# Kernel tuning notes

Hardware: AMD Instinct MI355X
Metric: run time of the kernel (lower is better)

Reference implementation:

```python
import jax, jax.numpy as jnp
import numpy as np
import math

NUM_HEADS = 16
VEC_SIZE = 1024
HEAD_DIM = VEC_SIZE // NUM_HEADS


def setup_inputs() -> dict:
    key = jax.random.key(0)
    k1, k2, k3, k4, k5 = jax.random.split(key, 5)
    B, S, D = 2, 2048, VEC_SIZE
    x = jax.random.normal(k1, (B, S, D), dtype=jnp.float32)
    # Linear params, torch-style: y = x @ W.T + b
    s1 = 1.0 / math.sqrt(D)
    W_qkv = jax.random.uniform(k2, (3 * D, D), minval=-s1, maxval=s1, dtype=jnp.float32)
    b_qkv = jax.random.uniform(k3, (3 * D,), minval=-s1, maxval=s1, dtype=jnp.float32)
    W_out = jax.random.uniform(k4, (D, D), minval=-s1, maxval=s1, dtype=jnp.float32)
    b_out = jax.random.uniform(k5, (D,), minval=-s1, maxval=s1, dtype=jnp.float32)
    return {"x": x, "W_qkv": W_qkv, "b_qkv": b_qkv, "W_out": W_out, "b_out": b_out}


def reference(x, W_qkv, b_qkv, W_out, b_out):
    B, S, D = x.shape
    H, Hd = NUM_HEADS, HEAD_DIM
    qkv = x @ W_qkv.T + b_qkv                      # [B,S,3D]
    q, k, v = jnp.split(qkv, 3, axis=-1)
    # [B,S,H,Hd] -> [B,H,S,Hd]
    q = q.reshape(B, S, H, Hd).transpose(0, 2, 1, 3)
    k = k.reshape(B, S, H, Hd).transpose(0, 2, 1, 3)
    v = v.reshape(B, S, H, Hd).transpose(0, 2, 1, 3)
    weight = jnp.einsum('bhqd,bhkd->bhqk', q, k)   # [B,H,S,S]
    causal = jnp.triu(jnp.ones((S, S), dtype=bool), k=1)
    weight = jnp.where(causal, -jnp.inf, weight)
    weight = weight / jnp.sqrt(jnp.asarray(Hd, dtype=weight.dtype))
    weight = jax.nn.softmax(weight, axis=-1)
    out = jnp.einsum('bhqk,bhkd->bhqd', weight, v)  # [B,H,S,Hd]
    out = out.transpose(0, 2, 1, 3).reshape(B, S, D)
    return out @ W_out.T + b_out
```

## Files before the change

kernel.cpp:

```cpp
#include <hip/hip_runtime.h>
#include <hip/hip_bf16.h>

typedef __attribute__((ext_vector_type(8))) short short8;
typedef __attribute__((ext_vector_type(4))) short s4v;
typedef __attribute__((ext_vector_type(4))) float floatx4;

__device__ inline floatx4 mfma_bf16(short8 a, short8 b, floatx4 c) {
  return __builtin_amdgcn_mfma_f32_16x16x32_bf16(a, b, c, 0, 0, 0);
}
__device__ inline float exp2_fast(float x) { return __builtin_amdgcn_exp2f(x); }

__device__ inline short bf16s(float f) {
  __hip_bfloat16 h = __float2bfloat16(f);
  return *reinterpret_cast<short*>(&h);
}
__device__ inline float sbf16(short s) {
  return __bfloat162float(*reinterpret_cast<__hip_bfloat16*>(&s));
}

__device__ inline void gld16(__hip_bfloat16* lds, const __hip_bfloat16* g) {
  __builtin_amdgcn_global_load_lds(
      (const __attribute__((address_space(1))) void*)g,
      (__attribute__((address_space(3))) void*)lds, 16, 0, 0);
}

__global__ __launch_bounds__(256) void cvt_all(
    const float* __restrict__ x, const float* __restrict__ wqkv,
    const float* __restrict__ wout, __hip_bfloat16* __restrict__ xb,
    __hip_bfloat16* __restrict__ wqkvb, __hip_bfloat16* __restrict__ wob) {
  const int n1 = 4194304, n2 = 3145728;
  int i = (blockIdx.x * 256 + threadIdx.x) * 8;
  const float* src;
  __hip_bfloat16* dst;
  int off;
  if (i < n1) { src = x; dst = xb; off = i; }
  else if (i < n1 + n2) { src = wqkv; dst = wqkvb; off = i - n1; }
  else { src = wout; dst = wob; off = i - n1 - n2; }
  float4 a = *reinterpret_cast<const float4*>(src + off);
  float4 b = *reinterpret_cast<const float4*>(src + off + 4);
  __hip_bfloat16 t[8];
  t[0] = __float2bfloat16(a.x); t[1] = __float2bfloat16(a.y);
  t[2] = __float2bfloat16(a.z); t[3] = __float2bfloat16(a.w);
  t[4] = __float2bfloat16(b.x); t[5] = __float2bfloat16(b.y);
  t[6] = __float2bfloat16(b.z); t[7] = __float2bfloat16(b.w);
  *reinterpret_cast<short8*>(dst + off) = *reinterpret_cast<short8*>(t);
}

template<int TN, bool OUT_BF16>
__global__ __launch_bounds__(256) void gemm_bt(
    const __hip_bfloat16* __restrict__ A, const __hip_bfloat16* __restrict__ Bt,
    const float* __restrict__ bias, void* __restrict__ Cout,
    int M, int N, int K) {
  __shared__ __align__(16) __hip_bfloat16 As[128 * 64];
  __shared__ __align__(16) __hip_bfloat16 Bs[TN * 64];
  const int tid = threadIdx.x;
  const int wave = tid >> 6, lane = tid & 63, quad = lane >> 4, l15 = lane & 15;
  const int wm = (wave >> 1) * 64, wn = (wave & 1) * (TN / 2);
  const int m0 = blockIdx.y * 128, n0 = blockIdx.x * TN;
  const int NC = TN / 32;

  floatx4 acc[4][NC];
  for (int r = 0; r < 4; ++r)
    for (int c = 0; c < NC; ++c) acc[r][c] = (floatx4){0.f, 0.f, 0.f, 0.f};

  for (int k0 = 0; k0 < K; k0 += 64) {
    __syncthreads();
    for (int it = 0; it < 4; ++it) {
      int idx = it * 256 + tid;
      int row = idx >> 3, col = ((idx & 7) ^ (row & 7)) * 8;
      gld16(&As[idx * 8], A + (size_t)(m0 + row) * K + k0 + col);
    }
    for (int it = 0; it < TN * 64 / 2048; ++it) {
      int idx = it * 256 + tid;
      int row = idx >> 3, col = ((idx & 7) ^ (row & 7)) * 8;
      gld16(&Bs[idx * 8], Bt + (size_t)(n0 + row) * K + k0 + col);
    }
    __syncthreads();
    for (int ks = 0; ks < 2; ++ks) {
      short8 af[4], bf[NC];
      for (int r = 0; r < 4; ++r) {
        int row = wm + r * 16 + l15;
        af[r] = *reinterpret_cast<const short8*>(
            &As[row * 64 + (((ks * 4 + quad) ^ (l15 & 7)) * 8)]);
      }
      for (int c = 0; c < NC; ++c) {
        int row = wn + c * 16 + l15;
        bf[c] = *reinterpret_cast<const short8*>(
            &Bs[row * 64 + (((ks * 4 + quad) ^ (l15 & 7)) * 8)]);
      }
      for (int r = 0; r < 4; ++r)
        for (int c = 0; c < NC; ++c)
          acc[r][c] = mfma_bf16(af[r], bf[c], acc[r][c]);
    }
  }

  for (int c = 0; c < NC; ++c) {
    int gn = n0 + wn + c * 16 + l15;
    float bv = bias[gn];
    for (int r = 0; r < 4; ++r)
      for (int rg = 0; rg < 4; ++rg) {
        int gm = m0 + wm + r * 16 + quad * 4 + rg;
        float v = acc[r][c][rg] + bv;
        if (OUT_BF16)
          ((__hip_bfloat16*)Cout)[(size_t)gm * N + gn] = __float2bfloat16(v);
        else
          ((float*)Cout)[(size_t)gm * N + gn] = v;
      }
  }
}

__global__ __launch_bounds__(256, 4) void flash_attn(
    const __hip_bfloat16* __restrict__ qkv, __hip_bfloat16* __restrict__ out) {
  const int S = 2048, QKV = 3072;
  const int bx = blockIdx.x;
  const int g = (blockIdx.y >> 3) + 2 * blockIdx.z;
  int qt;
  if (g == 0)      qt = bx;
  else if (g == 1) qt = 31 - bx;
  else if (g == 2) qt = (bx + 8) & 31;
  else             qt = (23 - bx) & 31;
  const int h = blockIdx.y, b = blockIdx.z;
  const int q0 = qt * 64;
  __shared__ __align__(16) short Ps[64 * 64];
  __shared__ __align__(16) short Ks[2][64 * 64];
  __shared__ __align__(16) short Vts[2][64 * 64];
  const int tid = threadIdx.x;
  const int wave = tid >> 6, lane = tid & 63, quad = lane >> 4, l15 = lane & 15;
  const int rx = l15 & 7;
  const __hip_bfloat16* base = qkv + (size_t)b * S * QKV;
  const float c2 = 0.18033688011112042f;
  const floatx4 zero4 = {0.f, 0.f, 0.f, 0.f};

  const int j4 = (tid >> 4) * 4, d4 = (tid & 15) * 4;

  for (int it = 0; it < 2; ++it) {
    int v = tid + it * 256;
    int row = v >> 3, cb = v & 7;
    int colp = (cb ^ (row & 7)) * 8;
    gld16((__hip_bfloat16*)&Ks[0][v * 8],
          base + (size_t)row * QKV + 1024 + h * 64 + colp);
    short8 qv = *reinterpret_cast<const short8*>(
        base + (size_t)(q0 + row) * QKV + h * 64 + cb * 8);
    short qs[8];
    for (int e = 0; e < 8; ++e) qs[e] = bf16s(sbf16(qv[e]) * c2);
    *reinterpret_cast<short8*>(&Ps[row * 64 + colp]) = *reinterpret_cast<short8*>(qs);
  }
  {
    s4v vr[4];
    for (int jj = 0; jj < 4; ++jj)
      vr[jj] = *reinterpret_cast<const s4v*>(
          base + (size_t)(j4 + jj) * QKV + 2048 + h * 64 + d4);
    for (int e = 0; e < 4; ++e) {
      int d = d4 + e;
      int pb = (j4 >> 3) ^ (d & 7) ^ ((d >> 3) & 7);
      s4v w4 = {vr[0][e], vr[1][e], vr[2][e], vr[3][e]};
      *reinterpret_cast<s4v*>(&Vts[0][d * 64 + pb * 8 + (j4 & 7)]) = w4;
    }
  }
  __syncthreads();
  short8 aq[4][2];
  for (int t4 = 0; t4 < 4; ++t4)
    for (int s = 0; s < 2; ++s)
      aq[t4][s] = *reinterpret_cast<const short8*>(
          &Ps[(t4 * 16 + l15) * 64 + (((s * 4 + quad) ^ rx) * 8)]);
  __syncthreads();

  floatx4 o_acc[4];
  for (int m = 0; m < 4; ++m) o_acc[m] = zero4;
  float lsum4[4] = {0.f, 0.f, 0.f, 0.f};
  const int krow = 16 * wave + l15;

  for (int kt = 0; kt <= qt; ++kt) {
    const int cur = kt & 1, nb = cur ^ 1;
    const bool havenext = kt < qt;
    s4v vr[4];
    if (havenext) {
      const size_t r1 = (size_t)(kt + 1) * 64;
      for (int it = 0; it < 2; ++it) {
        int v = tid + it * 256;
        int row = v >> 3, cb = v & 7;
        int colp = (cb ^ (row & 7)) * 8;
        gld16((__hip_bfloat16*)&Ks[nb][v * 8],
              base + (r1 + row) * QKV + 1024 + h * 64 + colp);
      }
      for (int jj = 0; jj < 4; ++jj)
        vr[jj] = *reinterpret_cast<const s4v*>(
            base + (r1 + j4 + jj) * QKV + 2048 + h * 64 + d4);
    }

    short8 ak0 = *reinterpret_cast<const short8*>(
        &Ks[cur][krow * 64 + ((quad ^ rx) * 8)]);
    short8 ak1 = *reinterpret_cast<const short8*>(
        &Ks[cur][krow * 64 + (((4 + quad) ^ rx) * 8)]);
    floatx4 sc[4];
    for (int t4 = 0; t4 < 4; ++t4) {
      sc[t4] = mfma_bf16(ak0, aq[t4][0], zero4);
      sc[t4] = mfma_bf16(ak1, aq[t4][1], sc[t4]);
    }
    if (kt == qt) {
      int kloc = 16 * wave + quad * 4;
      for (int t4 = 0; t4 < 4; ++t4)
        for (int rg = 0; rg < 4; ++rg)
          if (kloc + rg > t4 * 16 + l15) sc[t4][rg] = -1e30f;
    }
    const int pcol = ((2 * wave + (quad >> 1)) ^ rx) * 8 + (quad & 1) * 4;
    for (int t4 = 0; t4 < 4; ++t4) {
      short pp[4];
      for (int rg = 0; rg < 4; ++rg) {
        float p = exp2_fast(sc[t4][rg]);
        lsum4[t4] += p;
        pp[rg] = bf16s(p);
      }
      *reinterpret_cast<s4v*>(&Ps[(t4 * 16 + l15) * 64 + pcol]) =
          *reinterpret_cast<s4v*>(pp);
    }
    __syncthreads();

    const int dg = 16 * wave + l15;
    for (int s = 0; s < 2; ++s) {
      int gsw = ((4 * s + quad) ^ (dg & 7) ^ ((dg >> 3) & 7)) * 8;
      short8 bv = *reinterpret_cast<const short8*>(&Vts[cur][dg * 64 + gsw]);
      for (int m = 0; m < 4; ++m) {
        short8 ap = *reinterpret_cast<const short8*>(
            &Ps[(m * 16 + l15) * 64 + (((4 * s + quad) ^ rx) * 8)]);
        o_acc[m] = mfma_bf16(ap, bv, o_acc[m]);
      }
    }

    if (havenext) {
      for (int e = 0; e < 4; ++e) {
        int d = d4 + e;
        int pb = (j4 >> 3) ^ (d & 7) ^ ((d >> 3) & 7);
        s4v w4 = {vr[0][e], vr[1][e], vr[2][e], vr[3][e]};
        *reinterpret_cast<s4v*>(&Vts[nb][d * 64 + pb * 8 + (j4 & 7)]) = w4;
      }
    }
    __syncthreads();
  }

  for (int t4 = 0; t4 < 4; ++t4) {
    lsum4[t4] += __shfl_xor(lsum4[t4], 16);
    lsum4[t4] += __shfl_xor(lsum4[t4], 32);
  }
  float* Lf = (float*)Ps;
  if (quad == 0)
    for (int t4 = 0; t4 < 4; ++t4)
      Lf[wave * 64 + t4 * 16 + l15] = lsum4[t4];
  __syncthreads();
  if (tid < 64)
    Lf[256 + tid] = 1.0f / (Lf[tid] + Lf[64 + tid] + Lf[128 + tid] + Lf[192 + tid]);
  __syncthreads();

  const int dcol = h * 64 + 16 * wave + l15;
  for (int m = 0; m < 4; ++m)
    for (int rg = 0; rg < 4; ++rg) {
      int q = m * 16 + quad * 4 + rg;
      float inv = Lf[256 + q];
      out[(size_t)(b * S + q0 + q) * 1024 + dcol] =
          __float2bfloat16(o_acc[m][rg] * inv);
    }
}

extern "C" void kernel_launch(void* const* d_in, const int* in_sizes, int n_in,
                              void* d_out, int out_size, void* d_ws, size_t ws_size,
                              hipStream_t stream) {
  const float* x    = (const float*)d_in[0];
  const float* Wqkv = (const float*)d_in[1];
  const float* bqkv = (const float*)d_in[2];
  const float* Wout = (const float*)d_in[3];
  const float* bout = (const float*)d_in[4];
  float* out = (float*)d_out;

  const int BS = 2 * 2048;
  const int D = 1024;
  char* ws = (char*)d_ws;
  __hip_bfloat16* xb    = (__hip_bfloat16*)(ws);
  __hip_bfloat16* wqkvb = (__hip_bfloat16*)(ws + (size_t)8  * 1048576);
  __hip_bfloat16* wob   = (__hip_bfloat16*)(ws + (size_t)14 * 1048576);
  __hip_bfloat16* qkvb  = (__hip_bfloat16*)(ws + (size_t)16 * 1048576);
  __hip_bfloat16* attnb = (__hip_bfloat16*)(ws + (size_t)40 * 1048576);

  cvt_all<<<4096, 256, 0, stream>>>(x, Wqkv, Wout, xb, wqkvb, wob);

  gemm_bt<128, true><<<dim3(3072 / 128, BS / 128), 256, 0, stream>>>(
      xb, wqkvb, bqkv, qkvb, BS, 3 * D, D);

  flash_attn<<<dim3(32, 16, 2), 256, 0, stream>>>(qkvb, attnb);

  gemm_bt<64, false><<<dim3(1024 / 64, BS / 128), 256, 0, stream>>>(
      attnb, wob, bout, out, BS, D, D);
}
```

Baseline: 188.8 us.

## Software-pipeline flash attention: overlap PV of previous tile with QK of current

Restructures the attention loop so the P·V product for tile j-1 runs alongside the QK^T and softmax of tile j. Ps is double-buffered, and the V transpose write to LDS is deferred by one iteration. This cuts the per-iteration barriers from two to one and lets the scheduler interleave the two matrix phases. In exchange it uses more LDS and registers, so launch_bounds occupancy drops from 4 to 3 blocks per CU.

```diff
diff --git a/kernel.cpp b/kernel.cpp
--- a/kernel.cpp
+++ b/kernel.cpp
@@ -109,7 +109,7 @@
   }
 }
 
-__global__ __launch_bounds__(256, 4) void flash_attn(
+__global__ __launch_bounds__(256, 3) void flash_attn(
     const __hip_bfloat16* __restrict__ qkv, __hip_bfloat16* __restrict__ out) {
   const int S = 2048, QKV = 3072;
   const int bx = blockIdx.x;
@@ -121,7 +121,7 @@
   else             qt = (23 - bx) & 31;
   const int h = blockIdx.y, b = blockIdx.z;
   const int q0 = qt * 64;
-  __shared__ __align__(16) short Ps[64 * 64];
+  __shared__ __align__(16) short Ps[2][64 * 64];
   __shared__ __align__(16) short Ks[2][64 * 64];
   __shared__ __align__(16) short Vts[2][64 * 64];
   const int tid = threadIdx.x;
@@ -130,7 +130,6 @@
   const __hip_bfloat16* base = qkv + (size_t)b * S * QKV;
   const float c2 = 0.18033688011112042f;
   const floatx4 zero4 = {0.f, 0.f, 0.f, 0.f};
-
   const int j4 = (tid >> 4) * 4, d4 = (tid & 15) * 4;
 
   for (int it = 0; it < 2; ++it) {
@@ -143,66 +142,72 @@
         base + (size_t)(q0 + row) * QKV + h * 64 + cb * 8);
     short qs[8];
     for (int e = 0; e < 8; ++e) qs[e] = bf16s(sbf16(qv[e]) * c2);
-    *reinterpret_cast<short8*>(&Ps[row * 64 + colp]) = *reinterpret_cast<short8*>(qs);
-  }
-  {
-    s4v vr[4];
-    for (int jj = 0; jj < 4; ++jj)
-      vr[jj] = *reinterpret_cast<const s4v*>(
-          base + (size_t)(j4 + jj) * QKV + 2048 + h * 64 + d4);
-    for (int e = 0; e < 4; ++e) {
-      int d = d4 + e;
-      int pb = (j4 >> 3) ^ (d & 7) ^ ((d >> 3) & 7);
-      s4v w4 = {vr[0][e], vr[1][e], vr[2][e], vr[3][e]};
-      *reinterpret_cast<s4v*>(&Vts[0][d * 64 + pb * 8 + (j4 & 7)]) = w4;
-    }
-  }
+    *reinterpret_cast<short8*>(&Ps[1][row * 64 + colp]) = *reinterpret_cast<short8*>(qs);
+  }
+  s4v vr[4];
+  for (int jj = 0; jj < 4; ++jj)
+    vr[jj] = *reinterpret_cast<const s4v*>(
+        base + (size_t)(j4 + jj) * QKV + 2048 + h * 64 + d4);
   __syncthreads();
+
   short8 aq[4][2];
   for (int t4 = 0; t4 < 4; ++t4)
     for (int s = 0; s < 2; ++s)
       aq[t4][s] = *reinterpret_cast<const short8*>(
-          &Ps[(t4 * 16 + l15) * 64 + (((s * 4 + quad) ^ rx) * 8)]);
-  __syncthreads();
+          &Ps[1][(t4 * 16 + l15) * 64 + (((s * 4 + quad) ^ rx) * 8)]);
 
   floatx4 o_acc[4];
   for (int m = 0; m < 4; ++m) o_acc[m] = zero4;
   float lsum4[4] = {0.f, 0.f, 0.f, 0.f};
   const int krow = 16 * wave + l15;
-
-  for (int kt = 0; kt <= qt; ++kt) {
-    const int cur = kt & 1, nb = cur ^ 1;
-    const bool havenext = kt < qt;
-    s4v vr[4];
-    if (havenext) {
-      const size_t r1 = (size_t)(kt + 1) * 64;
+  const int dswz = (krow & 7) ^ ((krow >> 3) & 7);
+
+  for (int j = 0; j <= qt; ++j) {
+    const int cj = j & 1, pj = cj ^ 1;
+
+    s4v vrn[4];
+    if (j < qt) {
+      const size_t r1 = (size_t)(j + 1) * 64;
       for (int it = 0; it < 2; ++it) {
         int v = tid + it * 256;
         int row = v >> 3, cb = v & 7;
         int colp = (cb ^ (row & 7)) * 8;
-        gld16((__hip_bfloat16*)&Ks[nb][v * 8],
+        gld16((__hip_bfloat16*)&Ks[pj][v * 8],
               base + (r1 + row) * QKV + 1024 + h * 64 + colp);
       }
       for (int jj = 0; jj < 4; ++jj)
-        vr[jj] = *reinterpret_cast<const s4v*>(
+        vrn[jj] = *reinterpret_cast<const s4v*>(
             base + (r1 + j4 + jj) * QKV + 2048 + h * 64 + d4);
     }
 
+    if (j > 0) {
+      for (int s = 0; s < 2; ++s) {
+        short8 bv = *reinterpret_cast<const short8*>(
+            &Vts[pj][krow * 64 + (((4 * s + quad) ^ dswz) * 8)]);
+        for (int m = 0; m < 4; ++m) {
+          short8 ap = *reinterpret_cast<const short8*>(
+              &Ps[pj][(m * 16 + l15) * 64 + (((4 * s + quad) ^ rx) * 8)]);
+          o_acc[m] = mfma_bf16(ap, bv, o_acc[m]);
+        }
+      }
+    }
+
     short8 ak0 = *reinterpret_cast<const short8*>(
-        &Ks[cur][krow * 64 + ((quad ^ rx) * 8)]);
+        &Ks[cj][krow * 64 + ((quad ^ rx) * 8)]);
     short8 ak1 = *reinterpret_cast<const short8*>(
-        &Ks[cur][krow * 64 + (((4 + quad) ^ rx) * 8)]);
+        &Ks[cj][krow * 64 + (((4 + quad) ^ rx) * 8)]);
     floatx4 sc[4];
     for (int t4 = 0; t4 < 4; ++t4) {
       sc[t4] = mfma_bf16(ak0, aq[t4][0], zero4);
       sc[t4] = mfma_bf16(ak1, aq[t4][1], sc[t4]);
     }
-    if (kt == qt) {
+    if (j == qt) {
       int kloc = 16 * wave + quad * 4;
       for (int t4 = 0; t4 < 4; ++t4)
         for (int rg = 0; rg < 4; ++rg)
           if (kloc + rg > t4 * 16 + l15) sc[t4][rg] = -1e30f;
     }
+
     const int pcol = ((2 * wave + (quad >> 1)) ^ rx) * 8 + (quad & 1) * 4;
     for (int t4 = 0; t4 < 4; ++t4) {
       short pp[4];
@@ -211,38 +216,36 @@
         lsum4[t4] += p;
         pp[rg] = bf16s(p);
       }
-      *reinterpret_cast<s4v*>(&Ps[(t4 * 16 + l15) * 64 + pcol]) =
+      *reinterpret_cast<s4v*>(&Ps[cj][(t4 * 16 + l15) * 64 + pcol]) =
           *reinterpret_cast<s4v*>(pp);
     }
+
+    for (int e = 0; e < 4; ++e) {
+      int d = d4 + e;
+      int pb = (j4 >> 3) ^ (d & 7) ^ ((d >> 3) & 7);
+      s4v w4 = {vr[0][e], vr[1][e], vr[2][e], vr[3][e]};
+      *reinterpret_cast<s4v*>(&Vts[cj][d * 64 + pb * 8 + (j4 & 7)]) = w4;
+    }
+    for (int jj = 0; jj < 4; ++jj) vr[jj] = vrn[jj];
+
     __syncthreads();
-
-    const int dg = 16 * wave + l15;
-    for (int s = 0; s < 2; ++s) {
-      int gsw = ((4 * s + quad) ^ (dg & 7) ^ ((dg >> 3) & 7)) * 8;
-      short8 bv = *reinterpret_cast<const short8*>(&Vts[cur][dg * 64 + gsw]);
-      for (int m = 0; m < 4; ++m) {
-        short8 ap = *reinterpret_cast<const short8*>(
-            &Ps[(m * 16 + l15) * 64 + (((4 * s + quad) ^ rx) * 8)]);
-        o_acc[m] = mfma_bf16(ap, bv, o_acc[m]);
-      }
-    }
-
-    if (havenext) {
-      for (int e = 0; e < 4; ++e) {
-        int d = d4 + e;
-        int pb = (j4 >> 3) ^ (d & 7) ^ ((d >> 3) & 7);
-        s4v w4 = {vr[0][e], vr[1][e], vr[2][e], vr[3][e]};
-        *reinterpret_cast<s4v*>(&Vts[nb][d * 64 + pb * 8 + (j4 & 7)]) = w4;
-      }
-    }
-    __syncthreads();
-  }
-
+  }
+
+  const int pq = qt & 1;
+  for (int s = 0; s < 2; ++s) {
+    short8 bv = *reinterpret_cast<const short8*>(
+        &Vts[pq][krow * 64 + (((4 * s + quad) ^ dswz) * 8)]);
+    for (int m = 0; m < 4; ++m) {
+      short8 ap = *reinterpret_cast<const short8*>(
+          &Ps[pq][(m * 16 + l15) * 64 + (((4 * s + quad) ^ rx) * 8)]);
+      o_acc[m] = mfma_bf16(ap, bv, o_acc[m]);
+    }
+  }
   for (int t4 = 0; t4 < 4; ++t4) {
     lsum4[t4] += __shfl_xor(lsum4[t4], 16);
     lsum4[t4] += __shfl_xor(lsum4[t4], 32);
   }
-  float* Lf = (float*)Ps;
+  float* Lf = (float*)&Ps[pq ^ 1][0];
   if (quad == 0)
     for (int t4 = 0; t4 < 4; ++t4)
       Lf[wave * 64 + t4 * 16 + l15] = lsum4[t4];
@@ -251,13 +254,12 @@
     Lf[256 + tid] = 1.0f / (Lf[tid] + Lf[64 + tid] + Lf[128 + tid] + Lf[192 + tid]);
   __syncthreads();
 
-  const int dcol = h * 64 + 16 * wave + l15;
+  const int dcol = h * 64 + krow;
   for (int m = 0; m < 4; ++m)
     for (int rg = 0; rg < 4; ++rg) {
       int q = m * 16 + quad * 4 + rg;
-      float inv = Lf[256 + q];
       out[(size_t)(b * S + q0 + q) * 1024 + dcol] =
-          __float2bfloat16(o_acc[m][rg] * inv);
+          __float2bfloat16(o_acc[m][rg] * Lf[256 + q]);
     }
 }
 
```

Measured after the change: 192.8 us. 1.02x slower.
